# Optimization experiments

Hardware: AMD Instinct MI355X
Metric: run time of the kernel (lower is better)

## Reference

```python
import jax, jax.numpy as jnp
import numpy as np
import math

B, L, H, D, HID = 2, 1024, 16, 64, 1024  # batch, seq, heads, head_dim, hidden_size


def _rope_tables(seq_len, dim):
    inv_freq = 1.0 / (10000.0 ** (jnp.arange(0, dim, 2, dtype=jnp.float32) / dim))
    t = jnp.arange(seq_len, dtype=jnp.float32)
    freqs = jnp.outer(t, inv_freq)            # (L, D/2)
    emb = jnp.concatenate([freqs, freqs], -1)  # (L, D)
    return jnp.cos(emb), jnp.sin(emb)


def _rotate_half(x):
    x1, x2 = jnp.split(x, 2, axis=-1)
    return jnp.concatenate([-x2, x1], axis=-1)


def _apply_rope(x, cos, sin):
    # x: (B,H,L,D); cos/sin: (1,1,L,D)
    return x * cos + _rotate_half(x) * sin


def setup_inputs() -> dict:
    key = jax.random.key(0)
    ks = jax.random.split(key, 8)
    s = 0.02
    return {
        "x": jax.random.normal(ks[0], (B, L, HID), jnp.float32),
        "w_qkv": jax.random.normal(ks[1], (HID, 3 * H * D), jnp.float32) * s,
        "w_o": jax.random.normal(ks[2], (H * D, HID), jnp.float32) * s,
        "log_p": jax.random.normal(ks[3], (H, 1, 1), jnp.float32) * 0.02,
        "log_a": jax.random.normal(ks[4], (H, 1, 1), jnp.float32) * 0.02,
        "w1": jax.random.normal(ks[5], (2 * H, 2 * H), jnp.float32) * s,
        "b1": jnp.zeros((2 * H,), jnp.float32),
        "w2": jax.random.normal(ks[6], (2 * H, H), jnp.float32) * s,
        "b2": jnp.zeros((H,), jnp.float32),
    }


def _forward(x, w_qkv, w_o, log_p, log_a, w1, b1, w2, b2):
    Bx, Lx, _ = x.shape
    qkv = jnp.dot(x, w_qkv).reshape(Bx, Lx, 3, H, D)
    qkv = jnp.transpose(qkv, (2, 0, 3, 1, 4))  # (3,B,H,L,D)
    q, k, v = qkv[0], qkv[1], qkv[2]

    cos, sin = _rope_tables(Lx, D)
    cos, sin = cos[None, None], sin[None, None]
    q = _apply_rope(q, cos, sin)
    k = _apply_rope(k, cos, sin)

    scale = 1.0 / math.sqrt(D)
    scores = jnp.einsum('bhid,bhjd->bhij', q, k) * scale  # (B,H,L,L)

    # Kerple bias: -p * log1p(a * |m-n|), per head
    pos = jnp.arange(Lx, dtype=jnp.float32)
    dist = jnp.abs(pos[None, :] - pos[:, None])            # (L,L)
    p = jax.nn.softplus(log_p)
    a = jax.nn.softplus(log_a)
    kerple = -p * jnp.log1p(a * dist[None])                # (H,L,L)

    # DAPE MLP refinement over head channel
    attn_t = jnp.transpose(scores, (0, 2, 3, 1))           # (B,L,L,H)
    kerple_t = jnp.broadcast_to(jnp.transpose(kerple, (1, 2, 0))[None], attn_t.shape)
    combined = jnp.concatenate([attn_t, kerple_t], axis=-1)  # (B,L,L,2H)
    hdn = jax.nn.gelu(jnp.dot(combined, w1) + b1, approximate=False)
    refined = jnp.dot(hdn, w2) + b2                        # (B,L,L,H)
    refined = jnp.transpose(refined, (0, 3, 1, 2))         # (B,H,L,L)

    scores = scores + kerple[None] + refined

    causal = jnp.tril(jnp.ones((Lx, Lx), dtype=bool))
    scores = jnp.where(causal[None, None], scores, -jnp.inf)
    weights = jax.nn.softmax(scores, axis=-1)
    out = jnp.einsum('bhij,bhjd->bhid', weights, v)        # (B,H,L,D)
    out = jnp.transpose(out, (0, 2, 1, 3)).reshape(Bx, Lx, H * D)
    return jnp.dot(out, w_o)


def reference(x, w_qkv, w_o, log_p, log_a, w1, b1, w2, b2):
    return _forward(x, w_qkv, w_o, log_p, log_a, w1, b1, w2, b2)
```

## Files before the change

kernel.cpp:

```cpp
#include <hip/hip_runtime.h>
#include <math.h>

#define Bv 2
#define Lv 1024
#define Hv 16
#define Dv 64
#define HIDv 1024

typedef unsigned short u16;
typedef short bf16x8 __attribute__((ext_vector_type(8)));
typedef unsigned short u16x4 __attribute__((ext_vector_type(4)));
typedef float f32x4 __attribute__((ext_vector_type(4)));

__device__ __forceinline__ u16 f2b(float f) {
    union { float f; unsigned u; } v; v.f = f;
    return (u16)((v.u + 0x8000u) >> 16);
}
__device__ __forceinline__ float b2f(u16 h) {
    union { unsigned u; float f; } v; v.u = ((unsigned)h) << 16;
    return v.f;
}

__device__ __forceinline__ void gl2lds16(const u16* g, u16* l) {
    __builtin_amdgcn_global_load_lds(
        (const __attribute__((address_space(1))) unsigned int*)g,
        (__attribute__((address_space(3))) unsigned int*)l,
        16, 0, 0);
}

__device__ __forceinline__ float gelu_fast(float x) {
    float x2 = x * x;
    float inner = __builtin_fmaf(0.044715f * x2, x, x);
    float e = __expf(-1.5957691216057308f * inner);
    return x / (1.0f + e);
}

template<int BM, int BN, int WM, int WN, bool CBF16>
__global__ __launch_bounds__(256) void gemm_bt(
    const u16* __restrict__ A, const u16* __restrict__ B, void* __restrict__ Cv,
    int M, int N, int K, float alpha)
{
    constexpr int NW = BN / WN;
    constexpr int MI = WM / 16;
    constexpr int NI = WN / 16;
    constexpr int LDB = BN + 8;
    constexpr int LDF = BN + 4;
    __shared__ u16 As[BM * 32];
    __shared__ u16 Bs[BN * 32];
    __shared__ u16 Ctb[CBF16 ? BM * LDB : 1];
    __shared__ float Ctf[CBF16 ? 1 : BM * LDF];

    const int m0 = blockIdx.y * BM;
    const int n0 = blockIdx.x * BN;

    const int tid = threadIdx.x;
    const int lane = tid & 63;
    const int wave = tid >> 6;
    const int wm0 = (wave / NW) * WM;
    const int wn0 = (wave % NW) * WN;
    const int fr = lane & 15;
    const int fq = lane >> 4;

    f32x4 acc[MI][NI];
    #pragma unroll
    for (int i = 0; i < MI; ++i)
        #pragma unroll
        for (int j = 0; j < NI; ++j) acc[i][j] = (f32x4){0.f, 0.f, 0.f, 0.f};

    for (int k0 = 0; k0 < K; k0 += 32) {
        #pragma unroll
        for (int it = 0; it < BM / 64; ++it) {
            int cid = tid + it * 256;
            int r = cid >> 2, ch = cid & 3;
            gl2lds16(A + (long long)(m0 + r) * K + k0 + ch * 8, &As[cid * 8]);
        }
        #pragma unroll
        for (int it = 0; it < BN / 64; ++it) {
            int cid = tid + it * 256;
            int r = cid >> 2, ch = cid & 3;
            gl2lds16(B + (long long)(n0 + r) * K + k0 + ch * 8, &Bs[cid * 8]);
        }
        __syncthreads();
        bf16x8 af[MI], bfr[NI];
        #pragma unroll
        for (int i = 0; i < MI; ++i)
            af[i] = *(const bf16x8*)&As[(wm0 + i * 16 + fr) * 32 + fq * 8];
        #pragma unroll
        for (int j = 0; j < NI; ++j)
            bfr[j] = *(const bf16x8*)&Bs[(wn0 + j * 16 + fr) * 32 + fq * 8];
        #pragma unroll
        for (int i = 0; i < MI; ++i)
            #pragma unroll
            for (int j = 0; j < NI; ++j)
                acc[i][j] = __builtin_amdgcn_mfma_f32_16x16x32_bf16(
                    af[i], bfr[j], acc[i][j], 0, 0, 0);
        __syncthreads();
    }

    #pragma unroll
    for (int i = 0; i < MI; ++i)
        #pragma unroll
        for (int j = 0; j < NI; ++j)
            #pragma unroll
            for (int r = 0; r < 4; ++r) {
                int row = wm0 + i * 16 + fq * 4 + r;
                int col = wn0 + j * 16 + fr;
                float v = acc[i][j][r] * alpha;
                if (CBF16) Ctb[row * LDB + col] = f2b(v);
                else       Ctf[row * LDF + col] = v;
            }
    __syncthreads();
    if (CBF16) {
        constexpr int CPR = BN / 8;
        #pragma unroll
        for (int c = 0; c < (BM * BN) / (8 * 256); ++c) {
            int cid = tid + c * 256;
            int row = cid / CPR, kc = cid % CPR;
            *(bf16x8*)((u16*)Cv + (long long)(m0 + row) * N + n0 + kc * 8) =
                *(const bf16x8*)&Ctb[row * LDB + kc * 8];
        }
    } else {
        constexpr int CPR = BN / 4;
        #pragma unroll
        for (int c = 0; c < (BM * BN) / (4 * 256); ++c) {
            int cid = tid + c * 256;
            int row = cid / CPR, kc = cid % CPR;
            *(float4*)((float*)Cv + (long long)(m0 + row) * N + n0 + kc * 4) =
                *(const float4*)&Ctf[row * LDF + kc * 4];
        }
    }
}

__global__ __launch_bounds__(256) void qk_direct(
    const u16* __restrict__ Q, const u16* __restrict__ K, u16* __restrict__ S)
{
    const int m0 = blockIdx.y * 128;
    const int n0 = blockIdx.x * 128;
    if (n0 > m0) return;
    const u16* A = Q + (long long)blockIdx.z * 65536;
    const u16* B = K + (long long)blockIdx.z * 65536;
    u16* C = S + (long long)blockIdx.z * 1048576;

    __shared__ u16 Ct[128 * 136];

    const int tid = threadIdx.x;
    const int lane = tid & 63;
    const int wave = tid >> 6;
    const int wm0 = (wave >> 1) * 64;
    const int wn0 = (wave & 1) * 64;
    const int fr = lane & 15;
    const int fq = lane >> 4;

    bf16x8 af[4][2], bfr[4][2];
    #pragma unroll
    for (int i = 0; i < 4; ++i)
        #pragma unroll
        for (int p = 0; p < 2; ++p) {
            af[i][p]  = *(const bf16x8*)&A[(m0 + wm0 + i * 16 + fr) * 64 + p * 32 + fq * 8];
            bfr[i][p] = *(const bf16x8*)&B[(n0 + wn0 + i * 16 + fr) * 64 + p * 32 + fq * 8];
        }

    f32x4 acc[4][4];
    #pragma unroll
    for (int i = 0; i < 4; ++i)
        #pragma unroll
        for (int j = 0; j < 4; ++j) acc[i][j] = (f32x4){0.f, 0.f, 0.f, 0.f};

    #pragma unroll
    for (int p = 0; p < 2; ++p)
        #pragma unroll
        for (int i = 0; i < 4; ++i)
            #pragma unroll
            for (int j = 0; j < 4; ++j)
                acc[i][j] = __builtin_amdgcn_mfma_f32_16x16x32_bf16(
                    af[i][p], bfr[j][p], acc[i][j], 0, 0, 0);

    #pragma unroll
    for (int i = 0; i < 4; ++i)
        #pragma unroll
        for (int j = 0; j < 4; ++j)
            #pragma unroll
            for (int r = 0; r < 4; ++r)
                Ct[(wm0 + i * 16 + fq * 4 + r) * 136 + wn0 + j * 16 + fr] =
                    f2b(acc[i][j][r] * 0.125f);
    __syncthreads();
    #pragma unroll
    for (int c = 0; c < 8; ++c) {
        int cid = tid + c * 256;
        int row = cid >> 4, kc = cid & 15;
        *(bf16x8*)&C[(long long)(m0 + row) * 1024 + n0 + kc * 8] =
            *(const bf16x8*)&Ct[row * 136 + kc * 8];
    }
}

__global__ __launch_bounds__(256) void pv_direct(
    const u16* __restrict__ W, const u16* __restrict__ VT, u16* __restrict__ O)
{
    const int m0 = blockIdx.x * 64;
    const int bh = blockIdx.y;
    const u16* A = W + (long long)bh * 1048576;
    const u16* B = VT + (long long)bh * 65536;
    const int b = bh >> 4, h = bh & 15;

    __shared__ u16 Ct[64 * 72];

    const int tid = threadIdx.x;
    const int lane = tid & 63;
    const int wave = tid >> 6;
    const int wm0 = (wave >> 1) * 32;
    const int wn0 = (wave & 1) * 32;
    const int fr = lane & 15;
    const int fq = lane >> 4;

    f32x4 acc[2][2];
    #pragma unroll
    for (int i = 0; i < 2; ++i)
        #pragma unroll
        for (int j = 0; j < 2; ++j) acc[i][j] = (f32x4){0.f, 0.f, 0.f, 0.f};

    const int Kend = m0 + 64;
    for (int k0 = 0; k0 < Kend; k0 += 64) {
        bf16x8 af[2][2], bfr[2][2];
        #pragma unroll
        for (int p = 0; p < 2; ++p) {
            #pragma unroll
            for (int i = 0; i < 2; ++i)
                af[p][i] = *(const bf16x8*)&A[(m0 + wm0 + i * 16 + fr) * 1024 + k0 + p * 32 + fq * 8];
            #pragma unroll
            for (int j = 0; j < 2; ++j)
                bfr[p][j] = *(const bf16x8*)&B[(wn0 + j * 16 + fr) * 1024 + k0 + p * 32 + fq * 8];
        }
        #pragma unroll
        for (int p = 0; p < 2; ++p)
            #pragma unroll
            for (int i = 0; i < 2; ++i)
                #pragma unroll
                for (int j = 0; j < 2; ++j)
                    acc[i][j] = __builtin_amdgcn_mfma_f32_16x16x32_bf16(
                        af[p][i], bfr[p][j], acc[i][j], 0, 0, 0);
    }

    #pragma unroll
    for (int i = 0; i < 2; ++i)
        #pragma unroll
        for (int j = 0; j < 2; ++j)
            #pragma unroll
            for (int r = 0; r < 4; ++r)
                Ct[(wm0 + i * 16 + fq * 4 + r) * 72 + wn0 + j * 16 + fr] =
                    f2b(acc[i][j][r]);
    __syncthreads();
    const long long ob = (long long)b * 1048576 + h * 64;
    #pragma unroll
    for (int c = 0; c < 2; ++c) {
        int cid = tid + c * 256;
        int row = cid >> 3, kc = cid & 7;
        *(bf16x8*)&O[ob + (long long)(m0 + row) * 1024 + kc * 8] =
            *(const bf16x8*)&Ct[row * 72 + kc * 8];
    }
}

__global__ __launch_bounds__(256) void prep(
    const float* __restrict__ x, u16* __restrict__ x_bf,
    const float* __restrict__ w_qkv, u16* __restrict__ wqkvT,
    const float* __restrict__ w_o, u16* __restrict__ woT,
    const float* __restrict__ log_p, const float* __restrict__ log_a,
    u16* __restrict__ ktab)
{
    __shared__ float tile[64][65];
    const int bid = blockIdx.x;
    const int tid = threadIdx.x;

    if (bid < 8192) {
        int i = bid * 256 + tid;
        x_bf[i] = f2b(x[i]);
        return;
    }
    if (bid >= 9216) {
        int idx = (bid - 9216) * 256 + tid;
        int h = idx & 15, dist = idx >> 4;
        float pp = log1pf(__expf(log_p[h]));
        float aa = log1pf(__expf(log_a[h]));
        ktab[idx] = f2b(-pp * log1pf(aa * (float)dist));
        return;
    }
    const float* src; u16* dst; int M, N, bx, by;
    if (bid < 8960) { int t = bid - 8192; bx = t % 48; by = t / 48; src = w_qkv; dst = wqkvT; M = 1024; N = 3072; }
    else            { int t = bid - 8960; bx = t % 16; by = t / 16; src = w_o;   dst = woT;   M = 1024; N = 1024; }
    const int m0 = by * 64, n0 = bx * 64;
    #pragma unroll
    for (int c = 0; c < 4; ++c) {
        int f = tid + c * 256;
        int r = f >> 4, cs = (f & 15) * 4;
        float4 v = *(const float4*)&src[(long long)(m0 + r) * N + n0 + cs];
        tile[r][cs] = v.x; tile[r][cs + 1] = v.y;
        tile[r][cs + 2] = v.z; tile[r][cs + 3] = v.w;
    }
    __syncthreads();
    int nl = tid >> 2, ms = (tid & 3) * 16;
    u16 outv[16];
    #pragma unroll
    for (int c = 0; c < 16; ++c) outv[c] = f2b(tile[ms + c][nl]);
    *(bf16x8*)&dst[(long long)(n0 + nl) * M + m0 + ms]     = *(bf16x8*)&outv[0];
    *(bf16x8*)&dst[(long long)(n0 + nl) * M + m0 + ms + 8] = *(bf16x8*)&outv[8];
}

__global__ __launch_bounds__(256) void rope_vt(
    const u16* __restrict__ qkv,
    u16* __restrict__ q, u16* __restrict__ k, u16* __restrict__ vT)
{
    __shared__ u16 tile[64][65];
    const int l0 = blockIdx.x * 64;
    const int bh = blockIdx.y;
    const int b = bh >> 4, h = bh & 15;
    const int tid = threadIdx.x;
    const int r = tid >> 2;
    const int cs = (tid & 3) * 16;
    const int l = l0 + r;
    const long long src = ((long long)(b * 1024 + l) * 3) * 1024 + h * 64;
    const long long qkbase = ((long long)bh * 1024 + l) * 64 + cs;

    float cv[16], sv[16];
    #pragma unroll
    for (int e = 0; e < 16; ++e) {
        int d = cs + e;
        float inv_freq = __expf((float)(d & 31) * -0.28782313662425574f);
        __sincosf((float)l * inv_freq, &sv[e], &cv[e]);
    }
    const int csp = cs ^ 32;
    const float sgn = (cs < 32) ? -1.0f : 1.0f;

    #pragma unroll
    for (int w = 0; w < 2; ++w) {
        const long long s0 = src + w * 1024;
        u16 xv[16], xp[16];
        *(bf16x8*)&xv[0] = *(const bf16x8*)&qkv[s0 + cs];
        *(bf16x8*)&xv[8] = *(const bf16x8*)&qkv[s0 + cs + 8];
        *(bf16x8*)&xp[0] = *(const bf16x8*)&qkv[s0 + csp];
        *(bf16x8*)&xp[8] = *(const bf16x8*)&qkv[s0 + csp + 8];
        u16 o[16];
        #pragma unroll
        for (int e = 0; e < 16; ++e)
            o[e] = f2b(b2f(xv[e]) * cv[e] + sgn * b2f(xp[e]) * sv[e]);
        u16* dst = w ? k : q;
        *(bf16x8*)&dst[qkbase]     = *(bf16x8*)&o[0];
        *(bf16x8*)&dst[qkbase + 8] = *(bf16x8*)&o[8];
    }

    *(bf16x8*)&tile[r][cs]     = *(const bf16x8*)&qkv[src + 2048 + cs];
    *(bf16x8*)&tile[r][cs + 8] = *(const bf16x8*)&qkv[src + 2048 + cs + 8];
    __syncthreads();
    int dl = tid >> 2, ls = (tid & 3) * 16;
    u16 outv[16];
    #pragma unroll
    for (int c = 0; c < 16; ++c) outv[c] = tile[ls + c][dl];
    u16* d = vT + (long long)bh * 65536 + dl * 1024 + l0 + ls;
    *(bf16x8*)&d[0] = *(bf16x8*)&outv[0];
    *(bf16x8*)&d[8] = *(bf16x8*)&outv[8];
}

#define LSTR 1044

__global__ __launch_bounds__(512) void dape_soft(
    u16* __restrict__ S, const u16* __restrict__ ktab,
    const float* __restrict__ w1, const float* __restrict__ b1,
    const float* __restrict__ w2, const float* __restrict__ b2)
{
    const int i = 1023 - blockIdx.x;
    const int b = blockIdx.y;

    __shared__ u16 logits[16 * LSTR];
    __shared__ u16 comb[512 * 36];
    __shared__ u16 hid[8][16 * 36];

    const int tid = threadIdx.x;
    const int lane = tid & 63;
    const int wave = tid >> 6;
    const int fr = lane & 15;
    const int fq = lane >> 4;

    bf16x8 B1a, B1b, B2f, Bid;
    #pragma unroll
    for (int e = 0; e < 8; ++e) {
        int c = fq * 8 + e;
        B1a[e] = (short)f2b(w1[c * 32 + fr]);
        B1b[e] = (short)f2b(w1[c * 32 + 16 + fr]);
        B2f[e] = (short)f2b(w2[c * 16 + fr]);
        Bid[e] = (short)((c == fr || c == 16 + fr) ? 0x3F80 : 0);
    }
    const float b1a = b1[fr], b1b = b1[16 + fr], b2v = b2[fr];

    const long long sbase = (long long)b * 16 * 1048576 + (long long)i * 1024;
    const int nchunk = (i >> 9) + 1;

    for (int c = 0; c < nchunk; ++c) {
        const int j = c * 512 + tid;
        {
            u16 row[32];
            #pragma unroll
            for (int h = 0; h < 16; ++h)
                row[h] = S[sbase + (long long)h * 1048576 + j];
            const int dist = (i - j > 0) ? (i - j) : 0;
            *(bf16x8*)&row[16] = *(const bf16x8*)&ktab[dist * 16];
            *(bf16x8*)&row[24] = *(const bf16x8*)&ktab[dist * 16 + 8];
            #pragma unroll
            for (int qq = 0; qq < 4; ++qq)
                *(bf16x8*)&comb[tid * 36 + qq * 8] = *(bf16x8*)&row[qq * 8];
        }
        __syncthreads();

        for (int t = wave; t < 32; t += 8) {
            const int jt = c * 512 + t * 16;
            if (jt > i) continue;

            bf16x8 A1 = *(const bf16x8*)&comb[(t * 16 + fr) * 36 + fq * 8];
            f32x4 z = (f32x4){0.f, 0.f, 0.f, 0.f};
            f32x4 ac1a = __builtin_amdgcn_mfma_f32_16x16x32_bf16(A1, B1a, z, 0, 0, 0);
            f32x4 ac1b = __builtin_amdgcn_mfma_f32_16x16x32_bf16(A1, B1b, z, 0, 0, 0);
            f32x4 cres = __builtin_amdgcn_mfma_f32_16x16x32_bf16(
                A1, Bid, (f32x4){b2v, b2v, b2v, b2v}, 0, 0, 0);

            #pragma unroll
            for (int r = 0; r < 4; ++r) {
                float g0 = gelu_fast(ac1a[r] + b1a);
                float g1 = gelu_fast(ac1b[r] + b1b);
                hid[wave][(fq * 4 + r) * 36 + fr]      = f2b(g0);
                hid[wave][(fq * 4 + r) * 36 + 16 + fr] = f2b(g1);
            }
            bf16x8 A2 = *(const bf16x8*)&hid[wave][fr * 36 + fq * 8];
            f32x4 ac2 = __builtin_amdgcn_mfma_f32_16x16x32_bf16(A2, B2f, cres, 0, 0, 0);

            u16 o[4];
            #pragma unroll
            for (int r = 0; r < 4; ++r) o[r] = f2b(ac2[r]);
            *(u16x4*)&logits[fr * LSTR + jt + fq * 4] = *(u16x4*)o;
        }
        __syncthreads();
    }

    const int we = ((i >> 7) + 1) << 7;
    for (int hh = wave; hh < 16; hh += 8) {
        float vals[16];
        float mx = -3.0e38f;
        #pragma unroll
        for (int s = 0; s < 4; ++s) {
            u16x4 r4 = *(const u16x4*)&logits[hh * LSTR + lane * 4 + 256 * s];
            #pragma unroll
            for (int e = 0; e < 4; ++e) {
                int j = lane * 4 + 256 * s + e;
                float v = (j <= i) ? b2f(r4[e]) : -3.0e38f;
                vals[s * 4 + e] = v;
                mx = fmaxf(mx, v);
            }
        }
        #pragma unroll
        for (int off = 1; off < 64; off <<= 1)
            mx = fmaxf(mx, __shfl_xor(mx, off));
        float sm = 0.f;
        #pragma unroll
        for (int e = 0; e < 16; ++e) {
            float ev = (vals[e] > -1.0e37f) ? __expf(vals[e] - mx) : 0.f;
            vals[e] = ev;
            sm += ev;
        }
        #pragma unroll
        for (int off = 1; off < 64; off <<= 1)
            sm += __shfl_xor(sm, off);
        const float inv = 1.0f / sm;
        const long long hb = sbase + (long long)hh * 1048576;
        #pragma unroll
        for (int s = 0; s < 4; ++s) {
            int j0v = lane * 4 + 256 * s;
            if (j0v < we) {
                u16 o[4];
                #pragma unroll
                for (int e = 0; e < 4; ++e) o[e] = f2b(vals[s * 4 + e] * inv);
                *(u16x4*)&S[hb + j0v] = *(u16x4*)o;
            }
        }
    }
}

extern "C" void kernel_launch(void* const* d_in, const int* in_sizes, int n_in,
                              void* d_out, int out_size, void* d_ws, size_t ws_size,
                              hipStream_t stream)
{
    const float* x     = (const float*)d_in[0];
    const float* w_qkv = (const float*)d_in[1];
    const float* w_o   = (const float*)d_in[2];
    const float* log_p = (const float*)d_in[3];
    const float* log_a = (const float*)d_in[4];
    const float* w1    = (const float*)d_in[5];
    const float* b1    = (const float*)d_in[6];
    const float* w2    = (const float*)d_in[7];
    const float* b2    = (const float*)d_in[8];
    float* out = (float*)d_out;

    char* p = (char*)d_ws;
    u16* qkv_bf  = (u16*)p;    p += 6291456ll * 2;
    u16* x_bf    = (u16*)p;    p += 2097152ll * 2;
    u16* wqkvT   = (u16*)p;    p += 3145728ll * 2;
    u16* woT     = (u16*)p;    p += 1048576ll * 2;
    u16* q_bf    = (u16*)p;    p += 2097152ll * 2;
    u16* k_bf    = (u16*)p;    p += 2097152ll * 2;
    u16* vT      = (u16*)p;    p += 2097152ll * 2;
    u16* scores  = (u16*)p;    p += 33554432ll * 2;
    u16* attn_bf = (u16*)p;    p += 2097152ll * 2;
    u16* ktab    = (u16*)p;    p += 16384ll * 2;

    prep<<<9280, 256, 0, stream>>>(x, x_bf, w_qkv, wqkvT, w_o, woT,
                                   log_p, log_a, ktab);

    gemm_bt<64, 128, 32, 64, true><<<dim3(24, 32, 1), 256, 0, stream>>>(
        x_bf, wqkvT, qkv_bf, 2048, 3072, 1024, 1.0f);

    rope_vt<<<dim3(16, 32), 256, 0, stream>>>(qkv_bf, q_bf, k_bf, vT);

    qk_direct<<<dim3(8, 8, 32), 256, 0, stream>>>(q_bf, k_bf, scores);

    dape_soft<<<dim3(1024, 2), 512, 0, stream>>>(
        scores, ktab, w1, b1, w2, b2);

    pv_direct<<<dim3(16, 32), 256, 0, stream>>>(scores, vT, attn_bf);

    gemm_bt<64, 64, 32, 32, false><<<dim3(16, 32, 1), 256, 0, stream>>>(
        attn_bf, woT, out, 2048, 1024, 1024, 1.0f);
}
```

Baseline: 229.2 us.

## Fuse RoPE and V transpose into QKV GEMM epilogue with precomputed tables

Replaces the separate QKV GEMM plus rope_vt pass with one 128x128-tiled GEMM whose epilogue applies RoPE to Q/K via LDS staging and writes V transposed directly. This removes the round trip of the intermediate qkv buffer through global memory and one kernel launch. Cos/sin tables are now precomputed in prep, with the sign folded in. The tile change gives only 384 blocks, which may hurt occupancy or load balance, and V is written with scattered 8-byte stores.

```diff
diff --git a/kernel.cpp b/kernel.cpp
--- a/kernel.cpp
+++ b/kernel.cpp
@@ -33,6 +33,118 @@
     float inner = __builtin_fmaf(0.044715f * x2, x, x);
     float e = __expf(-1.5957691216057308f * inner);
     return x / (1.0f + e);
+}
+
+__global__ __launch_bounds__(256) void qkv_rope(
+    const u16* __restrict__ A, const u16* __restrict__ B,
+    const float* __restrict__ ctab, const float* __restrict__ stab,
+    u16* __restrict__ q, u16* __restrict__ k, u16* __restrict__ vT)
+{
+    __shared__ u16 As[128 * 32];
+    __shared__ u16 Bs[128 * 32];
+    __shared__ u16 Ct[128 * 136];
+
+    const int m0 = blockIdx.y * 128;
+    const int n0 = blockIdx.x * 128;
+    const int K = 1024;
+
+    const int tid = threadIdx.x;
+    const int lane = tid & 63;
+    const int wave = tid >> 6;
+    const int wm0 = (wave >> 1) * 64;
+    const int wn0 = (wave & 1) * 64;
+    const int fr = lane & 15;
+    const int fq = lane >> 4;
+
+    f32x4 acc[4][4];
+    #pragma unroll
+    for (int i = 0; i < 4; ++i)
+        #pragma unroll
+        for (int j = 0; j < 4; ++j) acc[i][j] = (f32x4){0.f, 0.f, 0.f, 0.f};
+
+    for (int k0 = 0; k0 < K; k0 += 32) {
+        #pragma unroll
+        for (int it = 0; it < 2; ++it) {
+            int cid = tid + it * 256;
+            int r = cid >> 2, ch = cid & 3;
+            gl2lds16(A + (long long)(m0 + r) * K + k0 + ch * 8, &As[cid * 8]);
+        }
+        #pragma unroll
+        for (int it = 0; it < 2; ++it) {
+            int cid = tid + it * 256;
+            int r = cid >> 2, ch = cid & 3;
+            gl2lds16(B + (long long)(n0 + r) * K + k0 + ch * 8, &Bs[cid * 8]);
+        }
+        __syncthreads();
+        bf16x8 af[4], bfr[4];
+        #pragma unroll
+        for (int i = 0; i < 4; ++i)
+            af[i] = *(const bf16x8*)&As[(wm0 + i * 16 + fr) * 32 + fq * 8];
+        #pragma unroll
+        for (int j = 0; j < 4; ++j)
+            bfr[j] = *(const bf16x8*)&Bs[(wn0 + j * 16 + fr) * 32 + fq * 8];
+        #pragma unroll
+        for (int i = 0; i < 4; ++i)
+            #pragma unroll
+            for (int j = 0; j < 4; ++j)
+                acc[i][j] = __builtin_amdgcn_mfma_f32_16x16x32_bf16(
+                    af[i], bfr[j], acc[i][j], 0, 0, 0);
+        __syncthreads();
+    }
+
+    const int b = m0 >> 10;
+
+    if (n0 >= 2048) {
+        #pragma unroll
+        for (int i = 0; i < 4; ++i)
+            #pragma unroll
+            for (int j = 0; j < 4; ++j) {
+                int vcol = (n0 - 2048) + wn0 + j * 16 + fr;
+                int head = vcol >> 6, d = vcol & 63;
+                int l = ((m0 + wm0 + i * 16 + fq * 4) & 1023);
+                u16 o[4];
+                #pragma unroll
+                for (int r = 0; r < 4; ++r) o[r] = f2b(acc[i][j][r]);
+                *(u16x4*)&vT[((long long)(b * 16 + head) * 64 + d) * 1024 + l] =
+                    *(u16x4*)o;
+            }
+        return;
+    }
+
+    #pragma unroll
+    for (int i = 0; i < 4; ++i)
+        #pragma unroll
+        for (int j = 0; j < 4; ++j)
+            #pragma unroll
+            for (int r = 0; r < 4; ++r)
+                Ct[(wm0 + i * 16 + fq * 4 + r) * 136 + wn0 + j * 16 + fr] =
+                    f2b(acc[i][j][r]);
+    __syncthreads();
+
+    u16* dst = (n0 >= 1024) ? k : q;
+    const int nh = n0 & 1023;
+    #pragma unroll
+    for (int c = 0; c < 8; ++c) {
+        int cid = tid + c * 256;
+        int row = cid >> 4, kc = cid & 15;
+        int l = (m0 + row) & 1023;
+        int head = (nh >> 6) + (kc >> 3);
+        int d0 = (kc & 7) * 8;
+        bf16x8 x  = *(const bf16x8*)&Ct[row * 136 + kc * 8];
+        bf16x8 xp = *(const bf16x8*)&Ct[row * 136 + (kc ^ 4) * 8];
+        float4 c0 = *(const float4*)&ctab[l * 64 + d0];
+        float4 c1 = *(const float4*)&ctab[l * 64 + d0 + 4];
+        float4 s0 = *(const float4*)&stab[l * 64 + d0];
+        float4 s1 = *(const float4*)&stab[l * 64 + d0 + 4];
+        float ct[8] = {c0.x, c0.y, c0.z, c0.w, c1.x, c1.y, c1.z, c1.w};
+        float st[8] = {s0.x, s0.y, s0.z, s0.w, s1.x, s1.y, s1.z, s1.w};
+        u16 o[8];
+        #pragma unroll
+        for (int e = 0; e < 8; ++e)
+            o[e] = f2b(b2f((u16)x[e]) * ct[e] + b2f((u16)xp[e]) * st[e]);
+        *(bf16x8*)&dst[((long long)(b * 16 + head) * 1024 + l) * 64 + d0] =
+            *(bf16x8*)o;
+    }
 }
 
 template<int BM, int BN, int WM, int WN, bool CBF16>
@@ -264,7 +376,7 @@
     const float* __restrict__ w_qkv, u16* __restrict__ wqkvT,
     const float* __restrict__ w_o, u16* __restrict__ woT,
     const float* __restrict__ log_p, const float* __restrict__ log_a,
-    u16* __restrict__ ktab)
+    u16* __restrict__ ktab, float* __restrict__ ctab, float* __restrict__ stab)
 {
     __shared__ float tile[64][65];
     const int bid = blockIdx.x;
@@ -273,6 +385,16 @@
     if (bid < 8192) {
         int i = bid * 256 + tid;
         x_bf[i] = f2b(x[i]);
+        return;
+    }
+    if (bid >= 9280) {
+        int idx = (bid - 9280) * 256 + tid;
+        int e = idx & 65535;
+        int l = e >> 6, d = e & 63;
+        float inv_freq = __expf((float)(d & 31) * -0.28782313662425574f);
+        float arg = (float)l * inv_freq;
+        if (idx < 65536) ctab[e] = __cosf(arg);
+        else             stab[e] = (d < 32) ? -__sinf(arg) : __sinf(arg);
         return;
     }
     if (bid >= 9216) {
@@ -302,60 +424,6 @@
     for (int c = 0; c < 16; ++c) outv[c] = f2b(tile[ms + c][nl]);
     *(bf16x8*)&dst[(long long)(n0 + nl) * M + m0 + ms]     = *(bf16x8*)&outv[0];
     *(bf16x8*)&dst[(long long)(n0 + nl) * M + m0 + ms + 8] = *(bf16x8*)&outv[8];
-}
-
-__global__ __launch_bounds__(256) void rope_vt(
-    const u16* __restrict__ qkv,
-    u16* __restrict__ q, u16* __restrict__ k, u16* __restrict__ vT)
-{
-    __shared__ u16 tile[64][65];
-    const int l0 = blockIdx.x * 64;
-    const int bh = blockIdx.y;
-    const int b = bh >> 4, h = bh & 15;
-    const int tid = threadIdx.x;
-    const int r = tid >> 2;
-    const int cs = (tid & 3) * 16;
-    const int l = l0 + r;
-    const long long src = ((long long)(b * 1024 + l) * 3) * 1024 + h * 64;
-    const long long qkbase = ((long long)bh * 1024 + l) * 64 + cs;
-
-    float cv[16], sv[16];
-    #pragma unroll
-    for (int e = 0; e < 16; ++e) {
-        int d = cs + e;
-        float inv_freq = __expf((float)(d & 31) * -0.28782313662425574f);
-        __sincosf((float)l * inv_freq, &sv[e], &cv[e]);
-    }
-    const int csp = cs ^ 32;
-    const float sgn = (cs < 32) ? -1.0f : 1.0f;
-
-    #pragma unroll
-    for (int w = 0; w < 2; ++w) {
-        const long long s0 = src + w * 1024;
-        u16 xv[16], xp[16];
-        *(bf16x8*)&xv[0] = *(const bf16x8*)&qkv[s0 + cs];
-        *(bf16x8*)&xv[8] = *(const bf16x8*)&qkv[s0 + cs + 8];
-        *(bf16x8*)&xp[0] = *(const bf16x8*)&qkv[s0 + csp];
-        *(bf16x8*)&xp[8] = *(const bf16x8*)&qkv[s0 + csp + 8];
-        u16 o[16];
-        #pragma unroll
-        for (int e = 0; e < 16; ++e)
-            o[e] = f2b(b2f(xv[e]) * cv[e] + sgn * b2f(xp[e]) * sv[e]);
-        u16* dst = w ? k : q;
-        *(bf16x8*)&dst[qkbase]     = *(bf16x8*)&o[0];
-        *(bf16x8*)&dst[qkbase + 8] = *(bf16x8*)&o[8];
-    }
-
-    *(bf16x8*)&tile[r][cs]     = *(const bf16x8*)&qkv[src + 2048 + cs];
-    *(bf16x8*)&tile[r][cs + 8] = *(const bf16x8*)&qkv[src + 2048 + cs + 8];
-    __syncthreads();
-    int dl = tid >> 2, ls = (tid & 3) * 16;
-    u16 outv[16];
-    #pragma unroll
-    for (int c = 0; c < 16; ++c) outv[c] = tile[ls + c][dl];
-    u16* d = vT + (long long)bh * 65536 + dl * 1024 + l0 + ls;
-    *(bf16x8*)&d[0] = *(bf16x8*)&outv[0];
-    *(bf16x8*)&d[8] = *(bf16x8*)&outv[8];
 }
 
 #define LSTR 1044
@@ -496,7 +564,6 @@
     float* out = (float*)d_out;
 
     char* p = (char*)d_ws;
-    u16* qkv_bf  = (u16*)p;    p += 6291456ll * 2;
     u16* x_bf    = (u16*)p;    p += 2097152ll * 2;
     u16* wqkvT   = (u16*)p;    p += 3145728ll * 2;
     u16* woT     = (u16*)p;    p += 1048576ll * 2;
@@ -506,14 +573,14 @@
     u16* scores  = (u16*)p;    p += 33554432ll * 2;
     u16* attn_bf = (u16*)p;    p += 2097152ll * 2;
     u16* ktab    = (u16*)p;    p += 16384ll * 2;
-
-    prep<<<9280, 256, 0, stream>>>(x, x_bf, w_qkv, wqkvT, w_o, woT,
-                                   log_p, log_a, ktab);
-
-    gemm_bt<64, 128, 32, 64, true><<<dim3(24, 32, 1), 256, 0, stream>>>(
-        x_bf, wqkvT, qkv_bf, 2048, 3072, 1024, 1.0f);
-
-    rope_vt<<<dim3(16, 32), 256, 0, stream>>>(qkv_bf, q_bf, k_bf, vT);
+    float* ctab  = (float*)p;  p += 65536ll * 4;
+    float* stab  = (float*)p;  p += 65536ll * 4;
+
+    prep<<<9792, 256, 0, stream>>>(x, x_bf, w_qkv, wqkvT, w_o, woT,
+                                   log_p, log_a, ktab, ctab, stab);
+
+    qkv_rope<<<dim3(24, 16), 256, 0, stream>>>(
+        x_bf, wqkvT, ctab, stab, q_bf, k_bf, vT);
 
     qk_direct<<<dim3(8, 8, 32), 256, 0, stream>>>(q_bf, k_bf, scores);
 
```

Result: faster. 224.1 us (-2.2%).
